# Kernel tuning notes

Hardware: AMD Instinct MI355X
Metric: run time of the kernel (lower is better)

## Reference

```python
import jax, jax.numpy as jnp
import numpy as np

K = 1024          # num_embeddings
D = 64            # embedding_dim
COMMIT = 0.25     # commitment_cost
B, C, T = 16, 64, 2048


def setup_inputs() -> dict:
    key = jax.random.key(0)
    k1, k2 = jax.random.split(key)
    inputs = jax.random.normal(k1, (B, C, T), dtype=jnp.float32)
    # nn.Embedding weight initialized uniform(-1/K, 1/K)
    weight = jax.random.uniform(k2, (K, D), dtype=jnp.float32,
                                minval=-1.0 / K, maxval=1.0 / K)
    return {"inputs": inputs, "weight": weight}


def reference(inputs, weight):
    # inputs: [B, C, T] -> [B, T, C] with C == D
    x = jnp.transpose(inputs, (0, 2, 1))          # [B, T, D]
    flat = x.reshape(-1, D)                        # [N, D], N = B*T

    distances = (jnp.sum(flat ** 2, axis=1, keepdims=True)
                 + jnp.sum(weight ** 2, axis=1)
                 - 2.0 * jnp.matmul(flat, weight.T))
    encoding_indices = jnp.argmin(distances, axis=1)          # [N]

    encodings = jax.nn.one_hot(encoding_indices, K, dtype=jnp.float32)  # [N, K]
    quantized = weight[encoding_indices].reshape(x.shape)     # [B, T, D] (== matmul(encodings, weight))

    e_latent_loss = jnp.mean((jax.lax.stop_gradient(quantized) - x) ** 2)
    q_latent_loss = jnp.mean((quantized - jax.lax.stop_gradient(x)) ** 2)
    loss = q_latent_loss + COMMIT * e_latent_loss

    # straight-through estimator
    quantized_st = x + jax.lax.stop_gradient(quantized - x)

    avg_probs = jnp.mean(encodings, axis=0)                   # [K]
    perplexity = jnp.exp(-jnp.sum(avg_probs * jnp.log(avg_probs + 1e-10)))

    quant_out = jnp.transpose(quantized_st, (0, 2, 1))        # [B, C, T]
    return loss, quant_out, perplexity, encodings
```

## Files before the change

### kernel.cpp

```cpp
#include <hip/hip_runtime.h>
#include <cstdint>
#include <cstddef>

#define K_CODES 1024
#define D_DIM   64
#define T_SZ    2048
#define N_ROWS  32768
#define BCT     2097152

typedef const __attribute__((address_space(1))) uint32_t* gp1_t;
typedef __attribute__((address_space(3))) uint32_t*       lp3_t;
typedef __attribute__((ext_vector_type(8))) short         short8;
typedef __attribute__((ext_vector_type(4))) float         f32x4;
typedef __attribute__((ext_vector_type(4))) int           i32x4;


__device__ __forceinline__ ushort bf16_rne(float f) {
    uint32_t u = __builtin_bit_cast(uint32_t, f);
    u += 0x7FFFu + ((u >> 16) & 1u);
    return (ushort)(u >> 16);
}
__device__ __forceinline__ float bf16_f(ushort h) {
    uint32_t u = ((uint32_t)h) << 16;
    return __builtin_bit_cast(float, u);
}

__global__ __launch_bounds__(256) void k_prep(const float* __restrict__ w,
                                              float* __restrict__ esq,
                                              ushort* __restrict__ wpack,
                                              int* __restrict__ hist,
                                              double* __restrict__ loss_sum) {
    const int gtid = blockIdx.x * 256 + threadIdx.x;
    const int k = gtid >> 3, grp = gtid & 7;
    if (gtid < K_CODES) hist[gtid] = 0;
    if (gtid == 0) loss_sum[0] = 0.0;
    const int ct = k >> 4, cl = k & 15;
    double s = 0.0;
#pragma unroll
    for (int jj = 0; jj < 8; ++jj) {
        const int d = grp * 8 + jj;
        const float x = w[k * 64 + d];
        s = fma((double)x, (double)x, s);
        const ushort hi = bf16_rne(x);
        const ushort lo = bf16_rne(x - bf16_f(hi));
        const int ks = d >> 5, g = (d >> 3) & 3, j = d & 7;
        const int lane = g * 16 + cl;
        const size_t base = ((size_t)(ct * 2 + ks)) * 2;
        wpack[((base + 0) * 64 + lane) * 8 + j] = hi;
        wpack[((base + 1) * 64 + lane) * 8 + j] = lo;
    }
    s += __shfl_xor(s, 1); s += __shfl_xor(s, 2); s += __shfl_xor(s, 4);
    if (grp == 0) esq[k] = (float)s;
}

__global__ __launch_bounds__(256, 2) void k_argmin(
        const float* __restrict__ in, const float* __restrict__ w,
        const float* __restrict__ esq, const ushort* __restrict__ wpack,
        int* __restrict__ hist, double* __restrict__ loss_sum,
        float* __restrict__ qout, float* __restrict__ enc) {
    __shared__ __align__(16) ushort lds_b[2][16384];
    __shared__ float  lds_esq[K_CODES];
    __shared__ int    smem_i1[64], smem_i2[64];
    __shared__ int    fin_s[64];
    __shared__ double redd[4];

    const int tid  = threadIdx.x;
    const int lane = tid & 63;
    const int wv   = tid >> 6;
    const int cl   = lane & 15;
    const int g    = lane >> 4;
    const int n0   = blockIdx.x * 64;
    const int b    = n0 >> 11;
    const int t0   = n0 & (T_SZ - 1);

#pragma unroll
    for (int r = 0; r < 4; ++r) lds_esq[r * 256 + tid] = esq[r * 256 + tid];

    const int t_row = t0 + wv * 16 + cl;
    short8 ah[2], al[2];
#pragma unroll
    for (int ks = 0; ks < 2; ++ks) {
        short8 h, l;
#pragma unroll
        for (int j = 0; j < 8; ++j) {
            const int d = ks * 32 + g * 8 + j;
            const float x = in[(size_t)b * 131072 + (size_t)d * T_SZ + t_row];
            const ushort hb = bf16_rne(x);
            h[j] = (short)hb;
            l[j] = (short)bf16_rne(x - bf16_f(hb));
        }
        ah[ks] = h;
        al[ks] = l;
    }

#define STAGEW(BUF, CH)                                                        \
    {                                                                          \
        _Pragma("unroll")                                                      \
        for (int r = 0; r < 8; ++r) {                                          \
            const int li = r * 256 + tid;                                      \
            const ushort* gsrc = wpack + (size_t)(CH)*16384 + (size_t)li * 8;  \
            ushort* ldst = &lds_b[BUF][li * 8];                                \
            __builtin_amdgcn_global_load_lds((gp1_t)gsrc, (lp3_t)ldst, 16, 0, 0);\
        }                                                                      \
    }

    STAGEW(0, 0)
    __syncthreads();

    f32x4 m1v = {-1e30f, -1e30f, -1e30f, -1e30f};
    f32x4 m2v = {-1e30f, -1e30f, -1e30f, -1e30f};
    i32x4 i1v = {0, 0, 0, 0};
    i32x4 i2v = {0, 0, 0, 0};

    int buf = 0;
    for (int ch = 0; ch < 8; ++ch) {
        if (ch < 7) STAGEW(buf ^ 1, ch + 1)
#pragma unroll
        for (int ctl = 0; ctl < 8; ++ctl) {
            const int ct = ch * 8 + ctl;
            const int c  = ct * 16 + cl;
            const float e2 = -0.5f * lds_esq[c];
            f32x4 accP = {e2, e2, e2, e2};
            f32x4 accQ = {0.f, 0.f, 0.f, 0.f};
#pragma unroll
            for (int ks = 0; ks < 2; ++ks) {
                const short8 bh = *(const short8*)&lds_b[buf][(((ctl * 2 + ks) * 2 + 0) * 64 + lane) * 8];
                const short8 bl = *(const short8*)&lds_b[buf][(((ctl * 2 + ks) * 2 + 1) * 64 + lane) * 8];
                accP = __builtin_amdgcn_mfma_f32_16x16x32_bf16(ah[ks], bh, accP, 0, 0, 0);
                accQ = __builtin_amdgcn_mfma_f32_16x16x32_bf16(ah[ks], bl, accQ, 0, 0, 0);
                accQ = __builtin_amdgcn_mfma_f32_16x16x32_bf16(al[ks], bh, accQ, 0, 0, 0);
            }
#pragma unroll
            for (int reg = 0; reg < 4; ++reg) {
                const float v = accP[reg] + accQ[reg];
                const bool gt1 = v > m1v[reg];
                const bool gt2 = v > m2v[reg];
                const float nm2 = gt1 ? m1v[reg] : (gt2 ? v : m2v[reg]);
                const int   ni2 = gt1 ? i1v[reg] : (gt2 ? c : i2v[reg]);
                m1v[reg] = gt1 ? v : m1v[reg];
                i1v[reg] = gt1 ? c : i1v[reg];
                m2v[reg] = nm2;
                i2v[reg] = ni2;
            }
        }
        __syncthreads();
        buf ^= 1;
    }

#pragma unroll
    for (int off = 1; off < 16; off <<= 1) {
#pragma unroll
        for (int reg = 0; reg < 4; ++reg) {
            const float pm1 = __shfl_xor(m1v[reg], off);
            const int   pi1 = __shfl_xor(i1v[reg], off);
            const float pm2 = __shfl_xor(m2v[reg], off);
            const int   pi2 = __shfl_xor(i2v[reg], off);
            const bool ours = (m1v[reg] > pm1) ||
                              (m1v[reg] == pm1 && i1v[reg] < pi1);
            float nm1, nm2; int ni1, ni2;
            if (ours) {
                nm1 = m1v[reg]; ni1 = i1v[reg];
                const bool pb = (pm1 > m2v[reg]) ||
                                (pm1 == m2v[reg] && pi1 < i2v[reg]);
                nm2 = pb ? pm1 : m2v[reg];
                ni2 = pb ? pi1 : i2v[reg];
            } else {
                nm1 = pm1; ni1 = pi1;
                const bool ob = (m1v[reg] > pm2) ||
                                (m1v[reg] == pm2 && i1v[reg] < pi2);
                nm2 = ob ? m1v[reg] : pm2;
                ni2 = ob ? i1v[reg] : pi2;
            }
            m1v[reg] = nm1; i1v[reg] = ni1;
            m2v[reg] = nm2; i2v[reg] = ni2;
        }
    }
    if (cl == 0) {
#pragma unroll
        for (int reg = 0; reg < 4; ++reg) {
            smem_i1[wv * 16 + g * 4 + reg] = i1v[reg];
            smem_i2[wv * 16 + g * 4 + reg] = i2v[reg];
        }
    }
    __syncthreads();

    {
        const int rloc = wv * 16 + (lane >> 2);
        const int quar = lane & 3;
        const int ii1 = smem_i1[rloc], ii2 = smem_i2[rloc];
        const int t = t0 + rloc;
        double v1 = 0.0, v2 = 0.0;
#pragma unroll
        for (int j = 0; j < 16; ++j) {
            const int d = quar * 16 + j;
            const double x = (double)in[(size_t)b * 131072 + (size_t)d * T_SZ + t];
            const double a  = (double)w[ii1 * 64 + d] - x;
            const double cc = (double)w[ii2 * 64 + d] - x;
            v1 = fma(a, a, v1);
            v2 = fma(cc, cc, v2);
        }
        v1 += __shfl_xor(v1, 1); v1 += __shfl_xor(v1, 2);
        v2 += __shfl_xor(v2, 1); v2 += __shfl_xor(v2, 2);
        if (quar == 0) {
            int fin;
            if (v1 < v2)      fin = ii1;
            else if (v2 < v1) fin = ii2;
            else              fin = (ii1 < ii2) ? ii1 : ii2;
            fin_s[rloc] = fin;
            atomicAdd(&hist[fin], 1);
        }
    }
    __syncthreads();

    float* lds_q = (float*)&lds_b[0][0];
#pragma unroll
    for (int r = 0; r < 16; ++r) {
        const int idx = r * 256 + tid;
        const int row = idx >> 6, d = idx & 63;
        lds_q[row * 65 + d] = w[fin_s[row] * 64 + d];
    }
    __syncthreads();

    double sq = 0.0;
#pragma unroll
    for (int it = 0; it < 16; ++it) {
        const int idx = it * 256 + tid;
        const int tt = idx & 63, d = idx >> 6;
        const size_t go = (size_t)b * 131072 + (size_t)d * T_SZ + t0 + tt;
        const float x = in[go];
        const float q = lds_q[tt * 65 + d];
        qout[go] = q;
        const double dd = (double)q - (double)x;
        sq = fma(dd, dd, sq);
    }
    for (int off = 32; off > 0; off >>= 1) sq += __shfl_down(sq, off);
    if (lane == 0) redd[wv] = sq;

#pragma unroll 1
    for (int rr = 0; rr < 16; ++rr) {
        const int rloc = wv * 16 + rr;
        const int f = fin_s[rloc];
        float* ebase = enc + (((size_t)(n0 + rloc)) << 10);
#pragma unroll
        for (int jj = 0; jj < 8; ++jj) {
            const int col = jj * 128 + lane * 2;
            float2 v;
            v.x = (col == f)     ? 1.0f : 0.0f;
            v.y = (col + 1 == f) ? 1.0f : 0.0f;
            *(float2*)(ebase + col) = v;
        }
    }

    __syncthreads();
    if (tid == 0) {
        double s = redd[0] + redd[1] + redd[2] + redd[3];
        atomicAdd(loss_sum, s);
    }
}

__global__ __launch_bounds__(256) void k_final(const int* __restrict__ hist,
                                               const double* __restrict__ loss_sum,
                                               float* __restrict__ out_loss,
                                               float* __restrict__ out_perp) {
    __shared__ double red[256];
    const int tid = threadIdx.x;
    double h = 0.0;
    for (int k = tid; k < K_CODES; k += 256) {
        const double p = (double)hist[k] / (double)N_ROWS;
        h += p * log(p + 1e-10);
    }
    red[tid] = h;
    __syncthreads();
#pragma unroll
    for (int st = 128; st > 0; st >>= 1) {
        if (tid < st) red[tid] += red[tid + st];
        __syncthreads();
    }
    if (tid == 0) {
        out_perp[0] = (float)exp(-red[0]);
        const double mean = loss_sum[0] / (double)BCT;
        out_loss[0] = (float)(1.25 * mean);
    }
}

extern "C" void kernel_launch(void* const* d_in, const int* in_sizes, int n_in,
                              void* d_out, int out_size, void* d_ws, size_t ws_size,
                              hipStream_t stream) {
    const float* in = (const float*)d_in[0];
    const float* w  = (const float*)d_in[1];

    float* out      = (float*)d_out;
    float* out_loss = out;
    float* out_q    = out + 1;
    float* out_perp = out + 1 + BCT;
    float* out_enc  = out + 2 + BCT;

    char*   ws       = (char*)d_ws;
    int*    ws_hist  = (int*)ws;
    double* ws_loss  = (double*)(ws + 4096);
    float*  ws_esq   = (float*)(ws + 8192);
    ushort* ws_wpack = (ushort*)(ws + 16384);

    k_prep  <<<32,  256, 0, stream>>>(w, ws_esq, ws_wpack, ws_hist, ws_loss);
    k_argmin<<<512, 256, 0, stream>>>(in, w, ws_esq, ws_wpack, ws_hist,
                                      ws_loss, out_q, out_enc);
    k_final <<<1,   256, 0, stream>>>(ws_hist, ws_loss, out_loss, out_perp);
}
```

Before: 188.7 us.

## Halve rows per block, split codebook across waves, fuse final reduction

Each block now handles 32 rows instead of 64. Its four waves split the work as two row tiles by two codebook halves, so 1024 blocks launch with half the LDS and twice the occupancy target. Each half keeps its own top-2 candidates, and four candidates per row are re-ranked in double precision. The separate final kernel is replaced by a last-block-done atomic counter, and s_setprio is added around the MFMA section. This raises parallelism and removes one launch, at the cost of more redundant staging per block and an extra candidate re-check.

```diff
diff --git a/kernel.cpp b/kernel.cpp
--- a/kernel.cpp
+++ b/kernel.cpp
@@ -29,11 +29,12 @@
                                               float* __restrict__ esq,
                                               ushort* __restrict__ wpack,
                                               int* __restrict__ hist,
-                                              double* __restrict__ loss_sum) {
+                                              double* __restrict__ loss_sum,
+                                              int* __restrict__ done) {
     const int gtid = blockIdx.x * 256 + threadIdx.x;
     const int k = gtid >> 3, grp = gtid & 7;
     if (gtid < K_CODES) hist[gtid] = 0;
-    if (gtid == 0) loss_sum[0] = 0.0;
+    if (gtid == 0) { loss_sum[0] = 0.0; done[0] = 0; }
     const int ct = k >> 4, cl = k & 15;
     double s = 0.0;
 #pragma unroll
@@ -53,30 +54,36 @@
     if (grp == 0) esq[k] = (float)s;
 }
 
-__global__ __launch_bounds__(256, 2) void k_argmin(
+__global__ __launch_bounds__(256, 4) void k_argmin(
         const float* __restrict__ in, const float* __restrict__ w,
         const float* __restrict__ esq, const ushort* __restrict__ wpack,
         int* __restrict__ hist, double* __restrict__ loss_sum,
-        float* __restrict__ qout, float* __restrict__ enc) {
-    __shared__ __align__(16) ushort lds_b[2][16384];
+        int* __restrict__ done, float* __restrict__ qout,
+        float* __restrict__ enc, float* __restrict__ out_loss,
+        float* __restrict__ out_perp) {
+    __shared__ __align__(16) ushort lds_b[2][8192];
     __shared__ float  lds_esq[K_CODES];
-    __shared__ int    smem_i1[64], smem_i2[64];
-    __shared__ int    fin_s[64];
+    __shared__ int    smem_c[32 * 4];
+    __shared__ int    fin_s[32];
     __shared__ double redd[4];
+    __shared__ int    last_s;
 
     const int tid  = threadIdx.x;
     const int lane = tid & 63;
     const int wv   = tid >> 6;
+    const int tile = wv & 1;
+    const int half = wv >> 1;
     const int cl   = lane & 15;
     const int g    = lane >> 4;
-    const int n0   = blockIdx.x * 64;
+    const int n0   = blockIdx.x * 32;
     const int b    = n0 >> 11;
     const int t0   = n0 & (T_SZ - 1);
+    const size_t bbase = (size_t)b * 131072;
 
 #pragma unroll
     for (int r = 0; r < 4; ++r) lds_esq[r * 256 + tid] = esq[r * 256 + tid];
 
-    const int t_row = t0 + wv * 16 + cl;
+    const int t_row = t0 + tile * 16 + cl;
     short8 ah[2], al[2];
 #pragma unroll
     for (int ks = 0; ks < 2; ++ks) {
@@ -84,7 +91,7 @@
 #pragma unroll
         for (int j = 0; j < 8; ++j) {
             const int d = ks * 32 + g * 8 + j;
-            const float x = in[(size_t)b * 131072 + (size_t)d * T_SZ + t_row];
+            const float x = in[bbase + (size_t)d * T_SZ + t_row];
             const ushort hb = bf16_rne(x);
             h[j] = (short)hb;
             l[j] = (short)bf16_rne(x - bf16_f(hb));
@@ -96,10 +103,10 @@
 #define STAGEW(BUF, CH)                                                        \
     {                                                                          \
         _Pragma("unroll")                                                      \
-        for (int r = 0; r < 8; ++r) {                                          \
-            const int li = r * 256 + tid;                                      \
-            const ushort* gsrc = wpack + (size_t)(CH)*16384 + (size_t)li * 8;  \
-            ushort* ldst = &lds_b[BUF][li * 8];                                \
+        for (int r = 0; r < 4; ++r) {                                          \
+            const int ct_src = (r < 2) ? (2 * (CH) + r) : (30 + 2 * (CH) + r); \
+            const ushort* gsrc = wpack + (size_t)ct_src * 2048 + (size_t)tid * 8;\
+            ushort* ldst = &lds_b[BUF][r * 2048 + tid * 8];                    \
             __builtin_amdgcn_global_load_lds((gp1_t)gsrc, (lp3_t)ldst, 16, 0, 0);\
         }                                                                      \
     }
@@ -113,19 +120,20 @@
     i32x4 i2v = {0, 0, 0, 0};
 
     int buf = 0;
-    for (int ch = 0; ch < 8; ++ch) {
-        if (ch < 7) STAGEW(buf ^ 1, ch + 1)
-#pragma unroll
-        for (int ctl = 0; ctl < 8; ++ctl) {
-            const int ct = ch * 8 + ctl;
-            const int c  = ct * 16 + cl;
+    for (int ch = 0; ch < 16; ++ch) {
+        if (ch < 15) STAGEW(buf ^ 1, ch + 1)
+        __builtin_amdgcn_s_setprio(1);
+#pragma unroll
+        for (int ctl = 0; ctl < 2; ++ctl) {
+            const int c = (half * 32 + 2 * ch + ctl) * 16 + cl;
+            const int slot = half * 2 + ctl;
             const float e2 = -0.5f * lds_esq[c];
             f32x4 accP = {e2, e2, e2, e2};
             f32x4 accQ = {0.f, 0.f, 0.f, 0.f};
 #pragma unroll
             for (int ks = 0; ks < 2; ++ks) {
-                const short8 bh = *(const short8*)&lds_b[buf][(((ctl * 2 + ks) * 2 + 0) * 64 + lane) * 8];
-                const short8 bl = *(const short8*)&lds_b[buf][(((ctl * 2 + ks) * 2 + 1) * 64 + lane) * 8];
+                const short8 bh = *(const short8*)&lds_b[buf][slot * 2048 + ((ks * 2 + 0) * 64 + lane) * 8];
+                const short8 bl = *(const short8*)&lds_b[buf][slot * 2048 + ((ks * 2 + 1) * 64 + lane) * 8];
                 accP = __builtin_amdgcn_mfma_f32_16x16x32_bf16(ah[ks], bh, accP, 0, 0, 0);
                 accQ = __builtin_amdgcn_mfma_f32_16x16x32_bf16(ah[ks], bl, accQ, 0, 0, 0);
                 accQ = __builtin_amdgcn_mfma_f32_16x16x32_bf16(al[ks], bh, accQ, 0, 0, 0);
@@ -143,6 +151,7 @@
                 i2v[reg] = ni2;
             }
         }
+        __builtin_amdgcn_s_setprio(0);
         __syncthreads();
         buf ^= 1;
     }
@@ -178,55 +187,60 @@
     if (cl == 0) {
 #pragma unroll
         for (int reg = 0; reg < 4; ++reg) {
-            smem_i1[wv * 16 + g * 4 + reg] = i1v[reg];
-            smem_i2[wv * 16 + g * 4 + reg] = i2v[reg];
-        }
-    }
-    __syncthreads();
-
+            const int row = tile * 16 + g * 4 + reg;
+            smem_c[row * 4 + half * 2 + 0] = i1v[reg];
+            smem_c[row * 4 + half * 2 + 1] = i2v[reg];
+        }
+    }
+    __syncthreads();
+
+    double* vcand = (double*)&lds_b[0][0];
     {
-        const int rloc = wv * 16 + (lane >> 2);
-        const int quar = lane & 3;
-        const int ii1 = smem_i1[rloc], ii2 = smem_i2[rloc];
-        const int t = t0 + rloc;
-        double v1 = 0.0, v2 = 0.0;
-#pragma unroll
-        for (int j = 0; j < 16; ++j) {
-            const int d = quar * 16 + j;
-            const double x = (double)in[(size_t)b * 131072 + (size_t)d * T_SZ + t];
-            const double a  = (double)w[ii1 * 64 + d] - x;
-            const double cc = (double)w[ii2 * 64 + d] - x;
-            v1 = fma(a, a, v1);
-            v2 = fma(cc, cc, v2);
-        }
-        v1 += __shfl_xor(v1, 1); v1 += __shfl_xor(v1, 2);
-        v2 += __shfl_xor(v2, 1); v2 += __shfl_xor(v2, 2);
-        if (quar == 0) {
-            int fin;
-            if (v1 < v2)      fin = ii1;
-            else if (v2 < v1) fin = ii2;
-            else              fin = (ii1 < ii2) ? ii1 : ii2;
-            fin_s[rloc] = fin;
-            atomicAdd(&hist[fin], 1);
-        }
+        const int cand = tid >> 1, dh = tid & 1;
+        const int row = cand >> 2, c4 = cand & 3;
+        const int idx = smem_c[row * 4 + c4];
+        const int t = t0 + row;
+        double v = 0.0;
+#pragma unroll
+        for (int j = 0; j < 32; ++j) {
+            const int d = dh * 32 + j;
+            const double x = (double)in[bbase + (size_t)d * T_SZ + t];
+            const double a = (double)w[idx * 64 + d] - x;
+            v = fma(a, a, v);
+        }
+        v += __shfl_xor(v, 1);
+        if (dh == 0) vcand[cand] = v;
+    }
+    __syncthreads();
+    if (tid < 32) {
+        const int row = tid;
+        double bv = vcand[row * 4]; int bi = smem_c[row * 4];
+#pragma unroll
+        for (int c4 = 1; c4 < 4; ++c4) {
+            const double v = vcand[row * 4 + c4];
+            const int   ii = smem_c[row * 4 + c4];
+            if (v < bv || (v == bv && ii < bi)) { bv = v; bi = ii; }
+        }
+        fin_s[row] = bi;
+        atomicAdd(&hist[bi], 1);
     }
     __syncthreads();
 
     float* lds_q = (float*)&lds_b[0][0];
 #pragma unroll
-    for (int r = 0; r < 16; ++r) {
-        const int idx = r * 256 + tid;
-        const int row = idx >> 6, d = idx & 63;
+    for (int r = 0; r < 8; ++r) {
+        const int li = r * 256 + tid;
+        const int row = li >> 6, d = li & 63;
         lds_q[row * 65 + d] = w[fin_s[row] * 64 + d];
     }
     __syncthreads();
 
     double sq = 0.0;
 #pragma unroll
-    for (int it = 0; it < 16; ++it) {
-        const int idx = it * 256 + tid;
-        const int tt = idx & 63, d = idx >> 6;
-        const size_t go = (size_t)b * 131072 + (size_t)d * T_SZ + t0 + tt;
+    for (int it = 0; it < 8; ++it) {
+        const int li = it * 256 + tid;
+        const int tt = li & 31, d = li >> 5;
+        const size_t go = bbase + (size_t)d * T_SZ + t0 + tt;
         const float x = in[go];
         const float q = lds_q[tt * 65 + d];
         qout[go] = q;
@@ -237,8 +251,8 @@
     if (lane == 0) redd[wv] = sq;
 
 #pragma unroll 1
-    for (int rr = 0; rr < 16; ++rr) {
-        const int rloc = wv * 16 + rr;
+    for (int rr = 0; rr < 8; ++rr) {
+        const int rloc = wv * 8 + rr;
         const int f = fin_s[rloc];
         float* ebase = enc + (((size_t)(n0 + rloc)) << 10);
 #pragma unroll
@@ -253,33 +267,35 @@
 
     __syncthreads();
     if (tid == 0) {
-        double s = redd[0] + redd[1] + redd[2] + redd[3];
+        const double s = redd[0] + redd[1] + redd[2] + redd[3];
         atomicAdd(loss_sum, s);
-    }
-}
-
-__global__ __launch_bounds__(256) void k_final(const int* __restrict__ hist,
-                                               const double* __restrict__ loss_sum,
-                                               float* __restrict__ out_loss,
-                                               float* __restrict__ out_perp) {
-    __shared__ double red[256];
-    const int tid = threadIdx.x;
-    double h = 0.0;
-    for (int k = tid; k < K_CODES; k += 256) {
-        const double p = (double)hist[k] / (double)N_ROWS;
-        h += p * log(p + 1e-10);
-    }
-    red[tid] = h;
-    __syncthreads();
-#pragma unroll
-    for (int st = 128; st > 0; st >>= 1) {
-        if (tid < st) red[tid] += red[tid + st];
+        __threadfence();
+        const int old = atomicAdd(done, 1);
+        last_s = (old == 1023) ? 1 : 0;
+    }
+    __syncthreads();
+
+    if (last_s) {
+        double* red = (double*)&lds_b[0][0];
+        double h = 0.0;
+#pragma unroll
+        for (int r = 0; r < 4; ++r) {
+            const int k = r * 256 + tid;
+            const int cnt = atomicAdd(&hist[k], 0);
+            const double p = (double)cnt / (double)N_ROWS;
+            h += p * log(p + 1e-10);
+        }
+        red[tid] = h;
         __syncthreads();
-    }
-    if (tid == 0) {
-        out_perp[0] = (float)exp(-red[0]);
-        const double mean = loss_sum[0] / (double)BCT;
-        out_loss[0] = (float)(1.25 * mean);
+        for (int st = 128; st > 0; st >>= 1) {
+            if (tid < st) red[tid] += red[tid + st];
+            __syncthreads();
+        }
+        if (tid == 0) {
+            out_perp[0] = (float)exp(-red[0]);
+            const double ls = atomicAdd(loss_sum, 0.0);
+            out_loss[0] = (float)(1.25 * (ls / (double)BCT));
+        }
     }
 }
 
@@ -298,11 +314,13 @@
     char*   ws       = (char*)d_ws;
     int*    ws_hist  = (int*)ws;
     double* ws_loss  = (double*)(ws + 4096);
+    int*    ws_done  = (int*)(ws + 4112);
     float*  ws_esq   = (float*)(ws + 8192);
     ushort* ws_wpack = (ushort*)(ws + 16384);
 
-    k_prep  <<<32,  256, 0, stream>>>(w, ws_esq, ws_wpack, ws_hist, ws_loss);
-    k_argmin<<<512, 256, 0, stream>>>(in, w, ws_esq, ws_wpack, ws_hist,
-                                      ws_loss, out_q, out_enc);
-    k_final <<<1,   256, 0, stream>>>(ws_hist, ws_loss, out_loss, out_perp);
-}
+    k_prep  <<<32,   256, 0, stream>>>(w, ws_esq, ws_wpack, ws_hist, ws_loss,
+                                       ws_done);
+    k_argmin<<<1024, 256, 0, stream>>>(in, w, ws_esq, ws_wpack, ws_hist,
+                                       ws_loss, ws_done, out_q, out_enc,
+                                       out_loss, out_perp);
+}
```

New measurement: 360.9 us. 1.91x slower.
